# Kernel optimization log

Measured on AMD Instinct MI355X. Metric: run time of the kernel, lower is better.

## Reference

```python
import jax, jax.numpy as jnp
import numpy as np

T = 100      # sequence length / output times
B = 2048     # batch
DT = 0.02    # euler step == spacing of ts -> one step per interval
CLAMP = 6.0
LOG2PI = float(np.log(2.0 * np.pi))
sp = jax.nn.softplus


def setup_inputs() -> dict:
    key = jax.random.key(0)
    ks = jax.random.split(key, 20)
    rn = lambda k, s, sc=1.0: jax.random.normal(k, s, dtype=jnp.float32) * sc
    inp = {}
    inp['xs'] = rn(ks[0], (T, B, 3, 50))
    inp['ts'] = jnp.arange(T, dtype=jnp.float32) * DT
    inp['eps0'] = rn(ks[1], (B, 6))
    inp['dW'] = rn(ks[2], (T - 1, B, 6)) * np.sqrt(DT)  # Brownian increments ~ N(0, dt)
    # encoder: 150->30->30->15
    inp['eW1'] = rn(ks[3], (150, 30), 150 ** -0.5); inp['eb1'] = jnp.zeros((30,), jnp.float32)
    inp['eW2'] = rn(ks[4], (30, 30), 30 ** -0.5);   inp['eb2'] = jnp.zeros((30,), jnp.float32)
    inp['eW3'] = rn(ks[5], (30, 15), 30 ** -0.5);   inp['eb3'] = jnp.zeros((15,), jnp.float32)
    # decoder: 6->30->30->100
    inp['dcW1'] = rn(ks[6], (6, 30), 6 ** -0.5);    inp['dcb1'] = jnp.zeros((30,), jnp.float32)
    inp['dcW2'] = rn(ks[7], (30, 30), 30 ** -0.5);  inp['dcb2'] = jnp.zeros((30,), jnp.float32)
    inp['dcW3'] = rn(ks[8], (30, 100), 30 ** -0.5); inp['dcb3'] = jnp.zeros((100,), jnp.float32)
    # f_net: (6+1+3)=10 -> 30 -> 6
    inp['fW1'] = rn(ks[9], (10, 30), 10 ** -0.5);   inp['fb1'] = jnp.zeros((30,), jnp.float32)
    inp['fW2'] = rn(ks[10], (30, 6), 30 ** -0.5);   inp['fb2'] = jnp.zeros((6,), jnp.float32)
    # h_net: (6+1)=7 -> 30 -> 6
    inp['hW1'] = rn(ks[11], (7, 30), 7 ** -0.5);    inp['hb1'] = jnp.zeros((30,), jnp.float32)
    inp['hW2'] = rn(ks[12], (30, 6), 30 ** -0.5);   inp['hb2'] = jnp.zeros((6,), jnp.float32)
    # 6 g_nets stacked: 2 -> 30 -> 1 (sigmoid)
    inp['gW1'] = rn(ks[13], (6, 2, 30), 2 ** -0.5); inp['gb1'] = jnp.zeros((6, 30), jnp.float32)
    inp['gW2'] = rn(ks[14], (6, 30, 1), 30 ** -0.5); inp['gb2'] = jnp.zeros((6, 1), jnp.float32)
    inp['pz0_mean'] = jnp.zeros((1, 6), jnp.float32)
    inp['pz0_logstd'] = jnp.zeros((1, 6), jnp.float32)
    return inp


def _forward(xs, ts, eps0, dW, eW1, eb1, eW2, eb2, eW3, eb3,
             dcW1, dcb1, dcW2, dcb2, dcW3, dcb3,
             fW1, fb1, fW2, fb2, hW1, hb1, hW2, hb2,
             gW1, gb1, gW2, gb2, pz0_mean, pz0_logstd):
    # ---- encoder on time-reversed xs ----
    xse = jnp.flip(xs, 0).reshape(T, B, 150)
    e = sp(xse @ eW1 + eb1)
    e = sp(e @ eW2 + eb2)
    e = e @ eW3 + eb3                         # [T,B,15]
    qz0_mean = e[-1, :, :6]
    qz0_logstd = e[-1, :, 6:12]
    ctx = jnp.flip(e[..., 12:15], 0)           # [T,B,3]

    z0 = qz0_mean + jnp.exp(jnp.clip(qz0_logstd, -CLAMP, CLAMP)) * eps0

    # ---- Euler-Maruyama with logqp (one step per ts interval) ----
    def step(z, sc):
        k, dWk = sc
        t = ts[k]
        dtk = ts[k + 1] - ts[k]
        c = ctx[jnp.minimum(k + 1, T - 1)]     # searchsorted(ts, t, right=True) clamped
        tb = jnp.broadcast_to(t, (B, 1)).astype(z.dtype)
        f = sp(jnp.concatenate([tb, z, c], 1) @ fW1 + fb1) @ fW2 + fb2
        h = sp(jnp.concatenate([tb, z], 1) @ hW1 + hb1) @ hW2 + hb2
        gin = jnp.stack([jnp.broadcast_to(t, (B, 6)).astype(z.dtype), z], -1)  # [B,6,2]
        gh = sp(jnp.einsum('bdi,dih->bdh', gin, gW1) + gb1)
        g = jax.nn.sigmoid(jnp.einsum('bdh,dho->bdo', gh, gW2) + gb2)[..., 0]  # [B,6]
        u = (f - h) / g
        logr = 0.5 * jnp.sum(u * u, axis=1) * dtk   # [B]
        zn = z + f * dtk + g * dWk
        return zn, (zn, logr)

    _, (zs_tail, log_ratio) = jax.lax.scan(step, z0, (jnp.arange(T - 1), dW))
    zs = jnp.concatenate([z0[None], zs_tail], 0)   # [T,B,6]

    # ---- decoder + likelihood ----
    d = sp(zs @ dcW1 + dcb1)
    d = sp(d @ dcW2 + dcb2)
    d = d @ dcW3 + dcb3                        # [T,B,100]
    xm, xl = d[..., :50], d[..., 50:]
    xsig = jnp.exp(jnp.clip(xl, -CLAMP, CLAMP))
    tgt = xs[:, :, -1, :]
    lp = -0.5 * ((tgt - xm) / xsig) ** 2 - jnp.log(xsig) - 0.5 * LOG2PI
    log_pxs = jnp.mean(jnp.sum(lp, axis=(0, 2)))

    # ---- KL(q(z0)||p(z0)) + path term ----
    sq = jnp.exp(jnp.clip(qz0_logstd, -CLAMP, CLAMP))
    spz = jnp.exp(jnp.clip(pz0_logstd, -CLAMP, CLAMP))
    kl = jnp.log(spz / sq) + (sq ** 2 + (qz0_mean - pz0_mean) ** 2) / (2.0 * spz ** 2) - 0.5
    logqp0 = jnp.mean(jnp.sum(kl, axis=1))
    logqp_path = jnp.mean(jnp.sum(log_ratio, axis=0))
    return log_pxs, logqp0 + logqp_path


def reference(xs, ts, eps0, dW, eW1, eb1, eW2, eb2, eW3, eb3,
              dcW1, dcb1, dcW2, dcb2, dcW3, dcb3,
              fW1, fb1, fW2, fb2, hW1, hb1, hW2, hb2,
              gW1, gb1, gW2, gb2, pz0_mean, pz0_logstd):
    return _forward(xs, ts, eps0, dW, eW1, eb1, eW2, eb2, eW3, eb3,
                    dcW1, dcb1, dcW2, dcb2, dcW3, dcb3,
                    fW1, fb1, fW2, fb2, hW1, hb1, hW2, hb2,
                    gW1, gb1, gW2, gb2, pz0_mean, pz0_logstd)
```

## Files before the change

kernel.cpp:

```cpp
#include <hip/hip_runtime.h>
#include <hip/hip_bf16.h>
#include <math.h>

#define Tn 100
#define Bn 2048

typedef int v2i __attribute__((ext_vector_type(2)));

__device__ __forceinline__ float sp_f(float x) {
    float e = __expf(-fabsf(x));
    return fmaxf(x, 0.f) + __logf(1.f + e);
}
__device__ __forceinline__ float clamp6(float x) {
    return fminf(fmaxf(x, -6.f), 6.f);
}
__device__ __forceinline__ float dpp_xor1(float x) {
    return __int_as_float(__builtin_amdgcn_mov_dpp(__float_as_int(x), 0xB1, 0xF, 0xF, 1));
}
__device__ __forceinline__ float dpp_xor2(float x) {
    return __int_as_float(__builtin_amdgcn_mov_dpp(__float_as_int(x), 0x4E, 0xF, 0xF, 1));
}
__device__ __forceinline__ float dpp_hmirror(float x) {
    return __int_as_float(__builtin_amdgcn_mov_dpp(__float_as_int(x), 0x141, 0xF, 0xF, 1));
}
__device__ __forceinline__ float dpp_ror8(float x) {
    return __int_as_float(__builtin_amdgcn_mov_dpp(__float_as_int(x), 0x128, 0xF, 0xF, 1));
}
template <int OFF>
__device__ __forceinline__ float swz(float x) {
    return __int_as_float(__builtin_amdgcn_ds_swizzle(__float_as_int(x), OFF));
}
__device__ __forceinline__ float xor16_sum(float x) {
#if __has_builtin(__builtin_amdgcn_permlane16_swap)
    v2i r = __builtin_amdgcn_permlane16_swap(__float_as_int(x), __float_as_int(x), false, false);
    return __int_as_float(r[0]) + __int_as_float(r[1]);
#else
    return x + swz<0x401F>(x);
#endif
}
__device__ __forceinline__ float other_half(float x) {
#if __has_builtin(__builtin_amdgcn_permlane32_swap)
    v2i r = __builtin_amdgcn_permlane32_swap(__float_as_int(x), __float_as_int(x), false, false);
    return (__int_as_float(r[0]) + __int_as_float(r[1])) - x;
#else
    return __shfl_xor(x, 32);
#endif
}

__device__ __forceinline__ void row2(float* ha, float* hb, const float* wrow,
                                     float va, float vb) {
#pragma unroll
    for (int q = 0; q < 7; ++q) {
        float4 wv = *(const float4*)(wrow + 4 * q);
        ha[4 * q + 0] = fmaf(va, wv.x, ha[4 * q + 0]);
        hb[4 * q + 0] = fmaf(vb, wv.x, hb[4 * q + 0]);
        ha[4 * q + 1] = fmaf(va, wv.y, ha[4 * q + 1]);
        hb[4 * q + 1] = fmaf(vb, wv.y, hb[4 * q + 1]);
        ha[4 * q + 2] = fmaf(va, wv.z, ha[4 * q + 2]);
        hb[4 * q + 2] = fmaf(vb, wv.z, hb[4 * q + 2]);
        ha[4 * q + 3] = fmaf(va, wv.w, ha[4 * q + 3]);
        hb[4 * q + 3] = fmaf(vb, wv.w, hb[4 * q + 3]);
    }
    float2 wt = *(const float2*)(wrow + 28);
    ha[28] = fmaf(va, wt.x, ha[28]);
    hb[28] = fmaf(vb, wt.x, hb[28]);
    ha[29] = fmaf(va, wt.y, ha[29]);
    hb[29] = fmaf(vb, wt.y, hb[29]);
}
__device__ __forceinline__ void dot30_2(const float* ha, const float* hb,
                                        const float* wrow, float& ra, float& rb) {
    float a0 = 0.f, a1 = 0.f, b0 = 0.f, b1 = 0.f;
#pragma unroll
    for (int q = 0; q < 7; ++q) {
        float4 wv = *(const float4*)(wrow + 4 * q);
        a0 = fmaf(ha[4 * q + 0], wv.x, a0);
        b0 = fmaf(hb[4 * q + 0], wv.x, b0);
        a1 = fmaf(ha[4 * q + 1], wv.y, a1);
        b1 = fmaf(hb[4 * q + 1], wv.y, b1);
        a0 = fmaf(ha[4 * q + 2], wv.z, a0);
        b0 = fmaf(hb[4 * q + 2], wv.z, b0);
        a1 = fmaf(ha[4 * q + 3], wv.w, a1);
        b1 = fmaf(hb[4 * q + 3], wv.w, b1);
    }
    float2 wt = *(const float2*)(wrow + 28);
    a0 = fmaf(ha[28], wt.x, a0);
    b0 = fmaf(hb[28], wt.x, b0);
    a1 = fmaf(ha[29], wt.y, a1);
    b1 = fmaf(hb[29], wt.y, b1);
    ra = a0 + a1; rb = b0 + b1;
}

#define ENC_LOAD2(b0, b1, base)                                               \
    _Pragma("unroll")                                                         \
    for (int i = 0; i < 5; ++i) {                                             \
        b0[i] = *(const float2*)(x0 + (base) + 2 * i);                        \
        b1[i] = *(const float2*)(x1 + (base) + 2 * i);                        \
    }
#define ENC_COMP2(b0, b1, base)                                               \
    _Pragma("unroll")                                                         \
    for (int i = 0; i < 5; ++i) {                                             \
        row2(h1a, h1b, &w[(base + 2 * i) * 32], b0[i].x, b1[i].x);            \
        row2(h1a, h1b, &w[(base + 2 * i + 1) * 32], b0[i].y, b1[i].y);        \
    }

__global__ __launch_bounds__(256) void enc_kernel(
    const float* __restrict__ xs,
    const float* __restrict__ eW1, const float* __restrict__ eb1,
    const float* __restrict__ eW2, const float* __restrict__ eb2,
    const float* __restrict__ eW3, const float* __restrict__ eb3,
    float* __restrict__ ctx, float* __restrict__ qm, float* __restrict__ qs)
{
    __shared__ float w[6292];
    for (int i = threadIdx.x; i < 4500; i += 256) w[(i / 30) * 32 + (i % 30)] = eW1[i];
    if (threadIdx.x < 30) w[4800 + threadIdx.x] = eb1[threadIdx.x];
    for (int i = threadIdx.x; i < 900; i += 256) w[4832 + (i / 30) * 32 + (i % 30)] = eW2[i];
    if (threadIdx.x < 30) w[5792 + threadIdx.x] = eb2[threadIdx.x];
    for (int i = threadIdx.x; i < 450; i += 256) w[5824 + i] = eW3[i];
    if (threadIdx.x < 15) w[6274 + threadIdx.x] = eb3[threadIdx.x];
    __syncthreads();

    int t = threadIdx.x;
    size_t base = (size_t)blockIdx.x * 512;
    size_t s0 = base + t, s1 = base + t + 256;
    const float* x0 = xs + s0 * 150;
    const float* x1 = xs + s1 * 150;

    float h1a[30], h1b[30];
#pragma unroll
    for (int j = 0; j < 30; ++j) { h1a[j] = w[4800 + j]; h1b[j] = h1a[j]; }

    float2 A0[5], A1[5], B0[5], B1[5];
    ENC_LOAD2(A0, A1, 0)
    ENC_LOAD2(B0, B1, 10)
    int fb = 0;
#pragma unroll 1
    for (int it = 0; it < 6; ++it) {
        ENC_COMP2(A0, A1, fb)
        ENC_LOAD2(A0, A1, fb + 20)
        ENC_COMP2(B0, B1, fb + 10)
        ENC_LOAD2(B0, B1, fb + 30)
        fb += 20;
    }
    ENC_COMP2(A0, A1, 120)
    ENC_LOAD2(A0, A1, 140)
    ENC_COMP2(B0, B1, 130)
    ENC_COMP2(A0, A1, 140)

#pragma unroll
    for (int j = 0; j < 30; ++j) { h1a[j] = sp_f(h1a[j]); h1b[j] = sp_f(h1b[j]); }

    float h2a[30], h2b[30];
#pragma unroll
    for (int j = 0; j < 30; ++j) { h2a[j] = w[5792 + j]; h2b[j] = h2a[j]; }
#pragma unroll
    for (int j1 = 0; j1 < 30; ++j1)
        row2(h2a, h2b, &w[4832 + j1 * 32], h1a[j1], h1b[j1]);
#pragma unroll
    for (int j = 0; j < 30; ++j) { h2a[j] = sp_f(h2a[j]); h2b[j] = sp_f(h2b[j]); }

    float oa12 = w[6274 + 12], oa13 = w[6274 + 13], oa14 = w[6274 + 14];
    float ob12 = oa12, ob13 = oa13, ob14 = oa14;
#pragma unroll
    for (int j2 = 0; j2 < 30; ++j2) {
        float w12 = w[5824 + j2 * 15 + 12];
        float w13 = w[5824 + j2 * 15 + 13];
        float w14 = w[5824 + j2 * 15 + 14];
        oa12 = fmaf(h2a[j2], w12, oa12); ob12 = fmaf(h2b[j2], w12, ob12);
        oa13 = fmaf(h2a[j2], w13, oa13); ob13 = fmaf(h2b[j2], w13, ob13);
        oa14 = fmaf(h2a[j2], w14, oa14); ob14 = fmaf(h2b[j2], w14, ob14);
    }
    float* cp0 = ctx + s0 * 3;
    cp0[0] = oa12; cp0[1] = oa13; cp0[2] = oa14;
    float* cp1 = ctx + s1 * 3;
    cp1[0] = ob12; cp1[1] = ob13; cp1[2] = ob14;

    if (blockIdx.x < 4) {
        float oa[12], ob[12];
#pragma unroll
        for (int j3 = 0; j3 < 12; ++j3) { oa[j3] = w[6274 + j3]; ob[j3] = oa[j3]; }
#pragma unroll
        for (int j2 = 0; j2 < 30; ++j2) {
            float hva = h2a[j2], hvb = h2b[j2];
#pragma unroll
            for (int j3 = 0; j3 < 12; ++j3) {
                float wv = w[5824 + j2 * 15 + j3];
                oa[j3] = fmaf(hva, wv, oa[j3]);
                ob[j3] = fmaf(hvb, wv, ob[j3]);
            }
        }
#pragma unroll
        for (int d = 0; d < 6; ++d) {
            qm[s0 * 6 + d] = oa[d]; qs[s0 * 6 + d] = oa[6 + d];
            qm[s1 * 6 + d] = ob[d]; qs[s1 * 6 + d] = ob[6 + d];
        }
    }
}

__global__ __launch_bounds__(128, 4) void scan_kernel(
    const float* __restrict__ ts, const float* __restrict__ dWall,
    const float* __restrict__ fW1, const float* __restrict__ fb1,
    const float* __restrict__ fW2, const float* __restrict__ fb2,
    const float* __restrict__ hW1, const float* __restrict__ hb1,
    const float* __restrict__ hW2, const float* __restrict__ hb2,
    const float* __restrict__ gW1, const float* __restrict__ gb1,
    const float* __restrict__ gW2, const float* __restrict__ gb2,
    const float* __restrict__ ctx,
    const float* __restrict__ qm, const float* __restrict__ qs,
    const float* __restrict__ eps0, const float* __restrict__ pm,
    const float* __restrict__ ps,
    float* __restrict__ zsb, float* __restrict__ acc)
{
    int tid = threadIdx.x;
    int lane = tid & 63;
    int b = blockIdx.x;
    bool isA = tid < 64;

    __shared__ float sRec[99 * 12];
    __shared__ float exF[2][12];
    __shared__ float exG[2][8];

    for (int i = tid; i < 99 * 3; i += 128) {
        int k = i / 3, e = i % 3;
        float2 v = *(const float2*)(dWall + ((size_t)k * Bn + b) * 6 + e * 2);
        *(float2*)&sRec[k * 12 + e * 2] = v;
    }
    for (int i = tid; i < 99 * 3; i += 128) {
        int k = i / 3, e = i % 3;
        sRec[k * 12 + 6 + e] = ctx[((size_t)(k + 1) * Bn + b) * 3 + e];
    }
    for (int i = tid; i < 99; i += 128) {
        float t0 = ts[i], t1 = ts[i + 1];
        sRec[i * 12 + 9]  = 0.f;
        sRec[i * 12 + 10] = t0;
        sRec[i * 12 + 11] = t1 - t0;
    }

    float z[6];
    float zq = 0.f;
    float wl1[10], b1w, wl2[6], fb2v[6], hb2v[6];
    float gwa[4], gwb[4], gw2v[4], gbb[4], gb2v = 0.f, wselq = 0.f;
    int dL = 0;

    if (isA) {
        bool lower = lane < 32;
        int j = lane & 31;
        int jc = (j < 30) ? j : 29;
        bool jvalid = (j < 30);
#pragma unroll
        for (int i = 0; i < 10; ++i)
            wl1[i] = lower ? fW1[i * 30 + jc] : (i < 7 ? hW1[i * 30 + jc] : 0.f);
        b1w = lower ? fb1[jc] : hb1[jc];
#pragma unroll
        for (int d = 0; d < 6; ++d)
            wl2[d] = jvalid ? (lower ? fW2[jc * 6 + d] : hW2[jc * 6 + d]) : 0.f;
#pragma unroll
        for (int d = 0; d < 6; ++d) { fb2v[d] = fb2[d]; hb2v[d] = hb2[d]; }
#pragma unroll
        for (int d = 0; d < 6; ++d) {
            float m = qm[b * 6 + d];
            float sq = __expf(clamp6(qs[b * 6 + d]));
            z[d] = fmaf(sq, eps0[b * 6 + d], m);
        }
        if (tid == 0) {
            float* zp = zsb + (size_t)b * 6;
            *(float2*)(zp)     = make_float2(z[0], z[1]);
            *(float2*)(zp + 2) = make_float2(z[2], z[3]);
            *(float2*)(zp + 4) = make_float2(z[4], z[5]);
        }
    } else {
        int dL8 = lane >> 3;
        dL = (dL8 < 6) ? dL8 : 0;
        wselq = (dL8 < 6) ? 0.0625f : 0.f;
        int s = lane & 7;
#pragma unroll
        for (int u = 0; u < 4; ++u) {
            int jj = s + 8 * u;
            bool ok = (dL8 < 6) && (jj < 30);
            gwa[u]  = ok ? gW1[dL * 60 + jj] : 0.f;
            gwb[u]  = ok ? gW1[dL * 60 + 30 + jj] : 0.f;
            gw2v[u] = ok ? gW2[dL * 30 + jj] : 0.f;
            gbb[u]  = ok ? gb1[dL * 30 + jj] : 0.f;
        }
        gb2v = gb2[dL];
        {
            float m = qm[b * 6 + dL];
            float sq = __expf(clamp6(qs[b * 6 + dL]));
            zq = fmaf(sq, eps0[b * 6 + dL], m);
        }
        if (tid == 64) {
            float klsum = 0.f;
#pragma unroll
            for (int d = 0; d < 6; ++d) {
                float m = qm[b * 6 + d];
                float sq = __expf(clamp6(qs[b * 6 + d]));
                float spz = __expf(clamp6(ps[d]));
                float dm = m - pm[d];
                klsum += __logf(spz / sq) + (sq * sq + dm * dm) / (2.f * spz * spz) - 0.5f;
            }
            atomicAdd(&acc[1], klsum);
        }
    }

    __syncthreads();

    float pacc = 0.f;

    for (int k = 0; k < Tn - 1; ++k) {
        int kb = k & 1;

        if (isA) {
            float4 r0 = *(float4*)&sRec[k * 12];
            float4 r1 = *(float4*)&sRec[k * 12 + 4];
            float4 r2 = *(float4*)&sRec[k * 12 + 8];
            float t = r2.z, dt = r2.w;

            float a = fmaf(t, wl1[0], b1w);
#pragma unroll
            for (int i = 0; i < 6; ++i) a = fmaf(z[i], wl1[1 + i], a);
            a = fmaf(r1.z, wl1[7], a);
            a = fmaf(r1.w, wl1[8], a);
            a = fmaf(r2.x, wl1[9], a);
            float hid = sp_f(a);

            float pp[6];
#pragma unroll
            for (int d = 0; d < 6; ++d) pp[d] = hid * wl2[d];
#pragma unroll
            for (int d = 0; d < 6; ++d) pp[d] += dpp_xor1(pp[d]);
#pragma unroll
            for (int d = 0; d < 6; ++d) pp[d] += dpp_xor2(pp[d]);
#pragma unroll
            for (int d = 0; d < 6; ++d) pp[d] += dpp_hmirror(pp[d]);
#pragma unroll
            for (int d = 0; d < 6; ++d) pp[d] += dpp_ror8(pp[d]);
#pragma unroll
            for (int d = 0; d < 6; ++d) pp[d] = xor16_sum(pp[d]);
            float fvv[6], dfh[6];
            bool lower = lane < 32;
#pragma unroll
            for (int d = 0; d < 6; ++d) {
                float oth = other_half(pp[d]);
                float fsum = lower ? pp[d] : oth;
                float hsum = lower ? oth : pp[d];
                fvv[d] = fsum + fb2v[d];
                dfh[d] = fvv[d] - (hsum + hb2v[d]);
            }
            if (lane == 0) {
                *(float4*)&exF[kb][0] = make_float4(fvv[0], fvv[1], fvv[2], fvv[3]);
                *(float4*)&exF[kb][4] = make_float4(fvv[4], fvv[5], dfh[0], dfh[1]);
                *(float4*)&exF[kb][8] = make_float4(dfh[2], dfh[3], dfh[4], dfh[5]);
            }

            __syncthreads();

            float4 g03 = *(float4*)&exG[kb][0];
            float2 g45 = *(float2*)&exG[kb][4];
            float gl[6] = { g03.x, g03.y, g03.z, g03.w, g45.x, g45.y };
            float dwv[6] = { r0.x, r0.y, r0.z, r0.w, r1.x, r1.y };
#pragma unroll
            for (int d = 0; d < 6; ++d)
                z[d] = fmaf(gl[d], dwv[d], fmaf(fvv[d], dt, z[d]));

            if (tid == 0) {
                float* zp = zsb + ((size_t)(k + 1) * Bn + b) * 6;
                *(float2*)(zp)     = make_float2(z[0], z[1]);
                *(float2*)(zp + 2) = make_float2(z[2], z[3]);
                *(float2*)(zp + 4) = make_float2(z[4], z[5]);
            }
        } else {
            float2 tdt = *(float2*)&sRec[k * 12 + 10];
            float t = tdt.x, dt = tdt.y;
            float dwq = sRec[k * 12 + dL];

            float ga = 0.f;
#pragma unroll
            for (int u = 0; u < 4; ++u) {
                float pre = fmaf(t, gwa[u], gbb[u]);
                pre = fmaf(zq, gwb[u], pre);
                ga = fmaf(sp_f(pre), gw2v[u], ga);
            }
            ga += dpp_xor1(ga);
            ga += dpp_xor2(ga);
            ga += dpp_hmirror(ga);
            float gacc = ga + gb2v;
            float e = __expf(-gacc);
            float rg = 1.f + e;
            float gval = __builtin_amdgcn_rcpf(rg);
            if ((lane & 7) == 0 && (lane >> 3) < 6)
                exG[kb][dL] = gval;

            __syncthreads();

            float fq  = exF[kb][dL];
            float dfq = exF[kb][6 + dL];
            float u = dfq * rg;
            pacc = fmaf(wselq * dt, u * u, pacc);
            zq = fmaf(gval, dwq, fmaf(fq, dt, zq));
        }
    }
    if (!isA) {
#pragma unroll
        for (int mm = 1; mm <= 32; mm <<= 1) pacc += __shfl_xor(pacc, mm);
        if (tid == 64) atomicAdd(&acc[2], pacc);
    }
}

#define DEC_TLOAD(b0, b1, base)                                               \
    _Pragma("unroll")                                                         \
    for (int i = 0; i < 5; ++i) {                                             \
        b0[i] = *(const float2*)(tg0 + (base) + 2 * i);                       \
        b1[i] = *(const float2*)(tg1 + (base) + 2 * i);                       \
    }
#define DEC_LCOMP(b0, b1, base)                                               \
    _Pragma("unroll")                                                         \
    for (int i = 0; i < 10; ++i) {                                            \
        int ff = (base) + i;                                                  \
        float dma, dmb, dla, dlb;                                             \
        dot30_2(h2a, h2b, &w[1216 + ff * 32], dma, dmb);                      \
        dot30_2(h2a, h2b, &w[1216 + (50 + ff) * 32], dla, dlb);               \
        float xma = w[4416 + ff] + dma, xmb = w[4416 + ff] + dmb;             \
        float cla = clamp6(w[4416 + 50 + ff] + dla);                          \
        float clb = clamp6(w[4416 + 50 + ff] + dlb);                          \
        float tva = (i & 1) ? b0[i >> 1].y : b0[i >> 1].x;                    \
        float tvb = (i & 1) ? b1[i >> 1].y : b1[i >> 1].x;                    \
        float ua = (tva - xma) * __expf(-cla);                                \
        float ub = (tvb - xmb) * __expf(-clb);                                \
        lpa += -0.5f * ua * ua - cla - 0.91893853320467274f;                  \
        lpb += -0.5f * ub * ub - clb - 0.91893853320467274f;                  \
    }

__global__ __launch_bounds__(256) void dec_kernel(
    const float* __restrict__ zsb, const float* __restrict__ xs,
    const float* __restrict__ dcW1, const float* __restrict__ dcb1,
    const float* __restrict__ dcW2, const float* __restrict__ dcb2,
    const float* __restrict__ dcW3, const float* __restrict__ dcb3,
    float* __restrict__ acc)
{
    __shared__ float w[4516];
    for (int i = threadIdx.x; i < 180; i += 256) w[(i / 30) * 32 + (i % 30)] = dcW1[i];
    if (threadIdx.x < 30) w[192 + threadIdx.x] = dcb1[threadIdx.x];
    for (int i = threadIdx.x; i < 900; i += 256) w[224 + (i / 30) * 32 + (i % 30)] = dcW2[i];
    if (threadIdx.x < 30) w[1184 + threadIdx.x] = dcb2[threadIdx.x];
    for (int i = threadIdx.x; i < 3000; i += 256) {
        int j2 = i / 100, j3 = i % 100;
        w[1216 + j3 * 32 + j2] = dcW3[i];
    }
    for (int i = threadIdx.x; i < 100; i += 256) w[4416 + i] = dcb3[i];
    __syncthreads();

    int t = threadIdx.x;
    size_t base = (size_t)blockIdx.x * 512;
    size_t s0 = base + t, s1 = base + t + 256;

    float za[6], zb[6];
    {
        const float* zp0 = zsb + s0 * 6;
        const float* zp1 = zsb + s1 * 6;
#pragma unroll
        for (int i = 0; i < 3; ++i) {
            float2 v0 = *(const float2*)(zp0 + 2 * i);
            float2 v1 = *(const float2*)(zp1 + 2 * i);
            za[2 * i] = v0.x; za[2 * i + 1] = v0.y;
            zb[2 * i] = v1.x; zb[2 * i + 1] = v1.y;
        }
    }

    float h1a[30], h1b[30];
#pragma unroll
    for (int j = 0; j < 30; ++j) { h1a[j] = w[192 + j]; h1b[j] = h1a[j]; }
#pragma unroll
    for (int i = 0; i < 6; ++i) row2(h1a, h1b, &w[i * 32], za[i], zb[i]);
#pragma unroll
    for (int j = 0; j < 30; ++j) { h1a[j] = sp_f(h1a[j]); h1b[j] = sp_f(h1b[j]); }

    float h2a[30], h2b[30];
#pragma unroll
    for (int j = 0; j < 30; ++j) { h2a[j] = w[1184 + j]; h2b[j] = h2a[j]; }
#pragma unroll
    for (int j1 = 0; j1 < 30; ++j1)
        row2(h2a, h2b, &w[224 + j1 * 32], h1a[j1], h1b[j1]);
#pragma unroll
    for (int j = 0; j < 30; ++j) { h2a[j] = sp_f(h2a[j]); h2b[j] = sp_f(h2b[j]); }

    const float* tg0 = xs + s0 * 150 + 100;
    const float* tg1 = xs + s1 * 150 + 100;
    float lpa = 0.f, lpb = 0.f;
    float2 TA0[5], TA1[5], TB0[5], TB1[5];
    DEC_TLOAD(TA0, TA1, 0)
    DEC_TLOAD(TB0, TB1, 10)
    DEC_LCOMP(TA0, TA1, 0)
    DEC_TLOAD(TA0, TA1, 20)
    DEC_LCOMP(TB0, TB1, 10)
    DEC_TLOAD(TB0, TB1, 30)
    DEC_LCOMP(TA0, TA1, 20)
    DEC_TLOAD(TA0, TA1, 40)
    DEC_LCOMP(TB0, TB1, 30)
    DEC_LCOMP(TA0, TA1, 40)

    float lpacc = lpa + lpb;
#pragma unroll
    for (int mm = 1; mm <= 32; mm <<= 1) lpacc += __shfl_xor(lpacc, mm);
    __shared__ float red[4];
    if ((threadIdx.x & 63) == 0) red[threadIdx.x >> 6] = lpacc;
    __syncthreads();
    if (threadIdx.x == 0) atomicAdd(&acc[0], red[0] + red[1] + red[2] + red[3]);
}

__global__ void final_kernel(const float* __restrict__ acc, float* __restrict__ out)
{
    out[0] = acc[0] * (1.f / (float)Bn);
    out[1] = (acc[1] + acc[2]) * (1.f / (float)Bn);
}

extern "C" void kernel_launch(void* const* d_in, const int* in_sizes, int n_in,
                              void* d_out, int out_size, void* d_ws, size_t ws_size,
                              hipStream_t stream)
{
    const float* xs   = (const float*)d_in[0];
    const float* ts   = (const float*)d_in[1];
    const float* eps0 = (const float*)d_in[2];
    const float* dW   = (const float*)d_in[3];
    const float* eW1  = (const float*)d_in[4];
    const float* eb1  = (const float*)d_in[5];
    const float* eW2  = (const float*)d_in[6];
    const float* eb2  = (const float*)d_in[7];
    const float* eW3  = (const float*)d_in[8];
    const float* eb3  = (const float*)d_in[9];
    const float* dcW1 = (const float*)d_in[10];
    const float* dcb1 = (const float*)d_in[11];
    const float* dcW2 = (const float*)d_in[12];
    const float* dcb2 = (const float*)d_in[13];
    const float* dcW3 = (const float*)d_in[14];
    const float* dcb3 = (const float*)d_in[15];
    const float* fW1  = (const float*)d_in[16];
    const float* fb1  = (const float*)d_in[17];
    const float* fW2  = (const float*)d_in[18];
    const float* fb2  = (const float*)d_in[19];
    const float* hW1  = (const float*)d_in[20];
    const float* hb1  = (const float*)d_in[21];
    const float* hW2  = (const float*)d_in[22];
    const float* hb2  = (const float*)d_in[23];
    const float* gW1  = (const float*)d_in[24];
    const float* gb1  = (const float*)d_in[25];
    const float* gW2  = (const float*)d_in[26];
    const float* gb2  = (const float*)d_in[27];
    const float* pm   = (const float*)d_in[28];
    const float* ps   = (const float*)d_in[29];

    float* ws  = (float*)d_ws;
    float* acc = ws;
    float* ctx = ws + 16;
    float* qm  = ctx + 614400;
    float* qs  = qm + 12288;
    float* zs  = qs + 12288;
    float* out = (float*)d_out;

    hipMemsetAsync(acc, 0, 16 * sizeof(float), stream);
    enc_kernel<<<400, 256, 0, stream>>>(xs, eW1, eb1, eW2, eb2, eW3, eb3, ctx, qm, qs);
    scan_kernel<<<2048, 128, 0, stream>>>(ts, dW, fW1, fb1, fW2, fb2, hW1, hb1,
                                          hW2, hb2, gW1, gb1, gW2, gb2, ctx,
                                          qm, qs, eps0, pm, ps, zs, acc);
    dec_kernel<<<400, 256, 0, stream>>>(zs, xs, dcW1, dcb1, dcW2, dcb2, dcW3, dcb3, acc);
    final_kernel<<<1, 1, 0, stream>>>(acc, out);
}
```

Before: 253.5 us.

## Use packed fp16 dot2 instructions for encoder and decoder MLP layers

Packs encoder and decoder weights and activations into fp16 pairs and replaces the fp32 FMA matrix products with v_dot2 fp16 instructions that accumulate in fp32, which halves the instruction count of the large layers. Shared memory layouts are rebuilt to hold the packed weights, and the encoder output layer is reorganised into dot products over transposed rows. This cuts ALU work and LDS traffic in the per-sample MLPs, at the cost of fp16 rounding of inputs, weights and hidden activations, which could push numerical error past tolerance.

Measured after the change: 244.0 us (median of 2 runs). 3.7% less time.

```diff
diff --git a/kernel.cpp b/kernel.cpp
--- a/kernel.cpp
+++ b/kernel.cpp
@@ -6,6 +6,7 @@
 #define Bn 2048
 
 typedef int v2i __attribute__((ext_vector_type(2)));
+typedef _Float16 h2v __attribute__((ext_vector_type(2)));
 
 __device__ __forceinline__ float sp_f(float x) {
     float e = __expf(-fabsf(x));
@@ -14,6 +15,20 @@
 __device__ __forceinline__ float clamp6(float x) {
     return fminf(fmaxf(x, -6.f), 6.f);
 }
+__device__ __forceinline__ unsigned int packh2(float a, float b) {
+    h2v h; h.x = (_Float16)a; h.y = (_Float16)b;
+    return __builtin_bit_cast(unsigned int, h);
+}
+__device__ __forceinline__ float dot2f(unsigned int a, unsigned int b, float c) {
+#if __has_builtin(__builtin_amdgcn_fdot2)
+    return __builtin_amdgcn_fdot2(__builtin_bit_cast(h2v, a),
+                                  __builtin_bit_cast(h2v, b), c, false);
+#else
+    h2v ha = __builtin_bit_cast(h2v, a), hb = __builtin_bit_cast(h2v, b);
+    return fmaf((float)ha.y, (float)hb.y, fmaf((float)ha.x, (float)hb.x, c));
+#endif
+}
+
 __device__ __forceinline__ float dpp_xor1(float x) {
     return __int_as_float(__builtin_amdgcn_mov_dpp(__float_as_int(x), 0xB1, 0xF, 0xF, 1));
 }
@@ -47,25 +62,25 @@
 #endif
 }
 
-__device__ __forceinline__ void row2(float* ha, float* hb, const float* wrow,
-                                     float va, float vb) {
+__device__ __forceinline__ void rowd2(float* ha, float* hb, const unsigned int* wrow,
+                                      unsigned int xa, unsigned int xb) {
 #pragma unroll
     for (int q = 0; q < 7; ++q) {
-        float4 wv = *(const float4*)(wrow + 4 * q);
-        ha[4 * q + 0] = fmaf(va, wv.x, ha[4 * q + 0]);
-        hb[4 * q + 0] = fmaf(vb, wv.x, hb[4 * q + 0]);
-        ha[4 * q + 1] = fmaf(va, wv.y, ha[4 * q + 1]);
-        hb[4 * q + 1] = fmaf(vb, wv.y, hb[4 * q + 1]);
-        ha[4 * q + 2] = fmaf(va, wv.z, ha[4 * q + 2]);
-        hb[4 * q + 2] = fmaf(vb, wv.z, hb[4 * q + 2]);
-        ha[4 * q + 3] = fmaf(va, wv.w, ha[4 * q + 3]);
-        hb[4 * q + 3] = fmaf(vb, wv.w, hb[4 * q + 3]);
-    }
-    float2 wt = *(const float2*)(wrow + 28);
-    ha[28] = fmaf(va, wt.x, ha[28]);
-    hb[28] = fmaf(vb, wt.x, hb[28]);
-    ha[29] = fmaf(va, wt.y, ha[29]);
-    hb[29] = fmaf(vb, wt.y, hb[29]);
+        uint4 wv = *(const uint4*)(wrow + 4 * q);
+        ha[4 * q + 0] = dot2f(xa, wv.x, ha[4 * q + 0]);
+        hb[4 * q + 0] = dot2f(xb, wv.x, hb[4 * q + 0]);
+        ha[4 * q + 1] = dot2f(xa, wv.y, ha[4 * q + 1]);
+        hb[4 * q + 1] = dot2f(xb, wv.y, hb[4 * q + 1]);
+        ha[4 * q + 2] = dot2f(xa, wv.z, ha[4 * q + 2]);
+        hb[4 * q + 2] = dot2f(xb, wv.z, hb[4 * q + 2]);
+        ha[4 * q + 3] = dot2f(xa, wv.w, ha[4 * q + 3]);
+        hb[4 * q + 3] = dot2f(xb, wv.w, hb[4 * q + 3]);
+    }
+    uint2 wt = *(const uint2*)(wrow + 28);
+    ha[28] = dot2f(xa, wt.x, ha[28]);
+    hb[28] = dot2f(xb, wt.x, hb[28]);
+    ha[29] = dot2f(xa, wt.y, ha[29]);
+    hb[29] = dot2f(xb, wt.y, hb[29]);
 }
 __device__ __forceinline__ void dot30_2(const float* ha, const float* hb,
                                         const float* wrow, float& ra, float& rb) {
@@ -89,6 +104,23 @@
     b1 = fmaf(hb[29], wt.y, b1);
     ra = a0 + a1; rb = b0 + b1;
 }
+__device__ __forceinline__ void dot16p_2(const unsigned int* pa, const unsigned int* pb,
+                                         const unsigned int* wrow, float& ra, float& rb) {
+    float a0 = 0.f, a1 = 0.f, b0 = 0.f, b1 = 0.f;
+#pragma unroll
+    for (int q = 0; q < 4; ++q) {
+        uint4 wv = *(const uint4*)(wrow + 4 * q);
+        a0 = dot2f(pa[4 * q + 0], wv.x, a0);
+        b0 = dot2f(pb[4 * q + 0], wv.x, b0);
+        a1 = dot2f(pa[4 * q + 1], wv.y, a1);
+        b1 = dot2f(pb[4 * q + 1], wv.y, b1);
+        a0 = dot2f(pa[4 * q + 2], wv.z, a0);
+        b0 = dot2f(pb[4 * q + 2], wv.z, b0);
+        a1 = dot2f(pa[4 * q + 3], wv.w, a1);
+        b1 = dot2f(pb[4 * q + 3], wv.w, b1);
+    }
+    ra = a0 + a1; rb = b0 + b1;
+}
 
 #define ENC_LOAD2(b0, b1, base)                                               \
     _Pragma("unroll")                                                         \
@@ -96,11 +128,12 @@
         b0[i] = *(const float2*)(x0 + (base) + 2 * i);                        \
         b1[i] = *(const float2*)(x1 + (base) + 2 * i);                        \
     }
-#define ENC_COMP2(b0, b1, base)                                               \
+#define ENC_COMP2(b0, b1, pb)                                                 \
     _Pragma("unroll")                                                         \
     for (int i = 0; i < 5; ++i) {                                             \
-        row2(h1a, h1b, &w[(base + 2 * i) * 32], b0[i].x, b1[i].x);            \
-        row2(h1a, h1b, &w[(base + 2 * i + 1) * 32], b0[i].y, b1[i].y);        \
+        unsigned int xa = packh2(b0[i].x, b0[i].y);                           \
+        unsigned int xb = packh2(b1[i].x, b1[i].y);                           \
+        rowd2(h1a, h1b, &wh1[((pb) + i) * 32], xa, xb);                       \
     }
 
 __global__ __launch_bounds__(256) void enc_kernel(
@@ -110,13 +143,29 @@
     const float* __restrict__ eW3, const float* __restrict__ eb3,
     float* __restrict__ ctx, float* __restrict__ qm, float* __restrict__ qs)
 {
-    __shared__ float w[6292];
-    for (int i = threadIdx.x; i < 4500; i += 256) w[(i / 30) * 32 + (i % 30)] = eW1[i];
-    if (threadIdx.x < 30) w[4800 + threadIdx.x] = eb1[threadIdx.x];
-    for (int i = threadIdx.x; i < 900; i += 256) w[4832 + (i / 30) * 32 + (i % 30)] = eW2[i];
-    if (threadIdx.x < 30) w[5792 + threadIdx.x] = eb2[threadIdx.x];
-    for (int i = threadIdx.x; i < 450; i += 256) w[5824 + i] = eW3[i];
-    if (threadIdx.x < 15) w[6274 + threadIdx.x] = eb3[threadIdx.x];
+    __shared__ __align__(16) unsigned int wh1[75 * 32];
+    __shared__ __align__(16) unsigned int wh2[15 * 32];
+    __shared__ __align__(16) float wf[555];
+
+    for (int i = threadIdx.x; i < 75 * 30; i += 256) {
+        int p = i / 30, j = i % 30;
+        wh1[p * 32 + j] = packh2(eW1[(2 * p) * 30 + j], eW1[(2 * p + 1) * 30 + j]);
+    }
+    for (int i = threadIdx.x; i < 15 * 30; i += 256) {
+        int p = i / 30, j = i % 30;
+        wh2[p * 32 + j] = packh2(eW2[(2 * p) * 30 + j], eW2[(2 * p + 1) * 30 + j]);
+    }
+    if (threadIdx.x < 30) wf[threadIdx.x] = eb1[threadIdx.x];
+    if (threadIdx.x >= 32 && threadIdx.x < 62) wf[30 + threadIdx.x - 32] = eb2[threadIdx.x - 32];
+    for (int i = threadIdx.x; i < 90; i += 256) {
+        int o = i / 30, j2 = i % 30;
+        wf[60 + o * 32 + j2] = eW3[j2 * 15 + 12 + o];
+    }
+    for (int i = threadIdx.x; i < 360; i += 256) {
+        int o = i / 30, j2 = i % 30;
+        wf[156 + o * 32 + j2] = eW3[j2 * 15 + o];
+    }
+    if (threadIdx.x >= 64 && threadIdx.x < 79) wf[540 + threadIdx.x - 64] = eb3[threadIdx.x - 64];
     __syncthreads();
 
     int t = threadIdx.x;
@@ -127,7 +176,7 @@
 
     float h1a[30], h1b[30];
 #pragma unroll
-    for (int j = 0; j < 30; ++j) { h1a[j] = w[4800 + j]; h1b[j] = h1a[j]; }
+    for (int j = 0; j < 30; ++j) { h1a[j] = wf[j]; h1b[j] = h1a[j]; }
 
     float2 A0[5], A1[5], B0[5], B1[5];
     ENC_LOAD2(A0, A1, 0)
@@ -135,63 +184,56 @@
     int fb = 0;
 #pragma unroll 1
     for (int it = 0; it < 6; ++it) {
-        ENC_COMP2(A0, A1, fb)
+        ENC_COMP2(A0, A1, fb / 2)
         ENC_LOAD2(A0, A1, fb + 20)
-        ENC_COMP2(B0, B1, fb + 10)
+        ENC_COMP2(B0, B1, fb / 2 + 5)
         ENC_LOAD2(B0, B1, fb + 30)
         fb += 20;
     }
-    ENC_COMP2(A0, A1, 120)
+    ENC_COMP2(A0, A1, 60)
     ENC_LOAD2(A0, A1, 140)
-    ENC_COMP2(B0, B1, 130)
-    ENC_COMP2(A0, A1, 140)
+    ENC_COMP2(B0, B1, 65)
+    ENC_COMP2(A0, A1, 70)
 
 #pragma unroll
     for (int j = 0; j < 30; ++j) { h1a[j] = sp_f(h1a[j]); h1b[j] = sp_f(h1b[j]); }
 
+    unsigned int p1a[15], p1b[15];
+#pragma unroll
+    for (int p = 0; p < 15; ++p) {
+        p1a[p] = packh2(h1a[2 * p], h1a[2 * p + 1]);
+        p1b[p] = packh2(h1b[2 * p], h1b[2 * p + 1]);
+    }
     float h2a[30], h2b[30];
 #pragma unroll
-    for (int j = 0; j < 30; ++j) { h2a[j] = w[5792 + j]; h2b[j] = h2a[j]; }
-#pragma unroll
-    for (int j1 = 0; j1 < 30; ++j1)
-        row2(h2a, h2b, &w[4832 + j1 * 32], h1a[j1], h1b[j1]);
+    for (int j = 0; j < 30; ++j) { h2a[j] = wf[30 + j]; h2b[j] = h2a[j]; }
+#pragma unroll
+    for (int p = 0; p < 15; ++p)
+        rowd2(h2a, h2b, &wh2[p * 32], p1a[p], p1b[p]);
 #pragma unroll
     for (int j = 0; j < 30; ++j) { h2a[j] = sp_f(h2a[j]); h2b[j] = sp_f(h2b[j]); }
 
-    float oa12 = w[6274 + 12], oa13 = w[6274 + 13], oa14 = w[6274 + 14];
-    float ob12 = oa12, ob13 = oa13, ob14 = oa14;
-#pragma unroll
-    for (int j2 = 0; j2 < 30; ++j2) {
-        float w12 = w[5824 + j2 * 15 + 12];
-        float w13 = w[5824 + j2 * 15 + 13];
-        float w14 = w[5824 + j2 * 15 + 14];
-        oa12 = fmaf(h2a[j2], w12, oa12); ob12 = fmaf(h2b[j2], w12, ob12);
-        oa13 = fmaf(h2a[j2], w13, oa13); ob13 = fmaf(h2b[j2], w13, ob13);
-        oa14 = fmaf(h2a[j2], w14, oa14); ob14 = fmaf(h2b[j2], w14, ob14);
+    float oa3[3], ob3[3];
+#pragma unroll
+    for (int o = 0; o < 3; ++o) {
+        float ra, rb;
+        dot30_2(h2a, h2b, &wf[60 + o * 32], ra, rb);
+        oa3[o] = wf[540 + 12 + o] + ra;
+        ob3[o] = wf[540 + 12 + o] + rb;
     }
     float* cp0 = ctx + s0 * 3;
-    cp0[0] = oa12; cp0[1] = oa13; cp0[2] = oa14;
+    cp0[0] = oa3[0]; cp0[1] = oa3[1]; cp0[2] = oa3[2];
     float* cp1 = ctx + s1 * 3;
-    cp1[0] = ob12; cp1[1] = ob13; cp1[2] = ob14;
+    cp1[0] = ob3[0]; cp1[1] = ob3[1]; cp1[2] = ob3[2];
 
     if (blockIdx.x < 4) {
-        float oa[12], ob[12];
-#pragma unroll
-        for (int j3 = 0; j3 < 12; ++j3) { oa[j3] = w[6274 + j3]; ob[j3] = oa[j3]; }
-#pragma unroll
-        for (int j2 = 0; j2 < 30; ++j2) {
-            float hva = h2a[j2], hvb = h2b[j2];
-#pragma unroll
-            for (int j3 = 0; j3 < 12; ++j3) {
-                float wv = w[5824 + j2 * 15 + j3];
-                oa[j3] = fmaf(hva, wv, oa[j3]);
-                ob[j3] = fmaf(hvb, wv, ob[j3]);
-            }
-        }
-#pragma unroll
-        for (int d = 0; d < 6; ++d) {
-            qm[s0 * 6 + d] = oa[d]; qs[s0 * 6 + d] = oa[6 + d];
-            qm[s1 * 6 + d] = ob[d]; qs[s1 * 6 + d] = ob[6 + d];
+#pragma unroll
+        for (int o = 0; o < 12; ++o) {
+            float ra, rb;
+            dot30_2(h2a, h2b, &wf[156 + o * 32], ra, rb);
+            float va = wf[540 + o] + ra, vb = wf[540 + o] + rb;
+            if (o < 6) { qm[s0 * 6 + o] = va; qm[s1 * 6 + o] = vb; }
+            else       { qs[s0 * 6 + o - 6] = va; qs[s1 * 6 + o - 6] = vb; }
         }
     }
 }
@@ -416,11 +458,11 @@
     for (int i = 0; i < 10; ++i) {                                            \
         int ff = (base) + i;                                                  \
         float dma, dmb, dla, dlb;                                             \
-        dot30_2(h2a, h2b, &w[1216 + ff * 32], dma, dmb);                      \
-        dot30_2(h2a, h2b, &w[1216 + (50 + ff) * 32], dla, dlb);               \
-        float xma = w[4416 + ff] + dma, xmb = w[4416 + ff] + dmb;             \
-        float cla = clamp6(w[4416 + 50 + ff] + dla);                          \
-        float clb = clamp6(w[4416 + 50 + ff] + dlb);                          \
+        dot16p_2(p2a, p2b, &wh3[ff * 16], dma, dmb);                          \
+        dot16p_2(p2a, p2b, &wh3[(50 + ff) * 16], dla, dlb);                   \
+        float xma = wd[256 + ff] + dma, xmb = wd[256 + ff] + dmb;             \
+        float cla = clamp6(wd[256 + 50 + ff] + dla);                          \
+        float clb = clamp6(wd[256 + 50 + ff] + dlb);                          \
         float tva = (i & 1) ? b0[i >> 1].y : b0[i >> 1].x;                    \
         float tvb = (i & 1) ? b1[i >> 1].y : b1[i >> 1].x;                    \
         float ua = (tva - xma) * __expf(-cla);                                \
@@ -436,16 +478,22 @@
     const float* __restrict__ dcW3, const float* __restrict__ dcb3,
     float* __restrict__ acc)
 {
-    __shared__ float w[4516];
-    for (int i = threadIdx.x; i < 180; i += 256) w[(i / 30) * 32 + (i % 30)] = dcW1[i];
-    if (threadIdx.x < 30) w[192 + threadIdx.x] = dcb1[threadIdx.x];
-    for (int i = threadIdx.x; i < 900; i += 256) w[224 + (i / 30) * 32 + (i % 30)] = dcW2[i];
-    if (threadIdx.x < 30) w[1184 + threadIdx.x] = dcb2[threadIdx.x];
-    for (int i = threadIdx.x; i < 3000; i += 256) {
-        int j2 = i / 100, j3 = i % 100;
-        w[1216 + j3 * 32 + j2] = dcW3[i];
-    }
-    for (int i = threadIdx.x; i < 100; i += 256) w[4416 + i] = dcb3[i];
+    __shared__ __align__(16) float wd[356];
+    __shared__ __align__(16) unsigned int wh2d[15 * 32];
+    __shared__ __align__(16) unsigned int wh3[100 * 16];
+
+    for (int i = threadIdx.x; i < 180; i += 256) wd[(i / 30) * 32 + (i % 30)] = dcW1[i];
+    if (threadIdx.x < 30) wd[192 + threadIdx.x] = dcb1[threadIdx.x];
+    if (threadIdx.x >= 32 && threadIdx.x < 62) wd[224 + threadIdx.x - 32] = dcb2[threadIdx.x - 32];
+    for (int i = threadIdx.x; i < 100; i += 256) wd[256 + i] = dcb3[i];
+    for (int i = threadIdx.x; i < 15 * 30; i += 256) {
+        int p = i / 30, j = i % 30;
+        wh2d[p * 32 + j] = packh2(dcW2[(2 * p) * 30 + j], dcW2[(2 * p + 1) * 30 + j]);
+    }
+    for (int i = threadIdx.x; i < 100 * 16; i += 256) {
+        int ff = i / 16, p = i % 16;
+        wh3[i] = (p < 15) ? packh2(dcW3[(2 * p) * 100 + ff], dcW3[(2 * p + 1) * 100 + ff]) : 0u;
+    }
     __syncthreads();
 
     int t = threadIdx.x;
@@ -467,20 +515,54 @@
 
     float h1a[30], h1b[30];
 #pragma unroll
-    for (int j = 0; j < 30; ++j) { h1a[j] = w[192 + j]; h1b[j] = h1a[j]; }
-#pragma unroll
-    for (int i = 0; i < 6; ++i) row2(h1a, h1b, &w[i * 32], za[i], zb[i]);
+    for (int j = 0; j < 30; ++j) { h1a[j] = wd[192 + j]; h1b[j] = h1a[j]; }
+#pragma unroll
+    for (int i = 0; i < 6; ++i) {
+        float via = za[i], vib = zb[i];
+        const float* wrow = &wd[i * 32];
+#pragma unroll
+        for (int q = 0; q < 7; ++q) {
+            float4 wv = *(const float4*)(wrow + 4 * q);
+            h1a[4 * q + 0] = fmaf(via, wv.x, h1a[4 * q + 0]);
+            h1b[4 * q + 0] = fmaf(vib, wv.x, h1b[4 * q + 0]);
+            h1a[4 * q + 1] = fmaf(via, wv.y, h1a[4 * q + 1]);
+            h1b[4 * q + 1] = fmaf(vib, wv.y, h1b[4 * q + 1]);
+            h1a[4 * q + 2] = fmaf(via, wv.z, h1a[4 * q + 2]);
+            h1b[4 * q + 2] = fmaf(vib, wv.z, h1b[4 * q + 2]);
+            h1a[4 * q + 3] = fmaf(via, wv.w, h1a[4 * q + 3]);
+            h1b[4 * q + 3] = fmaf(vib, wv.w, h1b[4 * q + 3]);
+        }
+        float2 wt = *(const float2*)(wrow + 28);
+        h1a[28] = fmaf(via, wt.x, h1a[28]);
+        h1b[28] = fmaf(vib, wt.x, h1b[28]);
+        h1a[29] = fmaf(via, wt.y, h1a[29]);
+        h1b[29] = fmaf(vib, wt.y, h1b[29]);
+    }
 #pragma unroll
     for (int j = 0; j < 30; ++j) { h1a[j] = sp_f(h1a[j]); h1b[j] = sp_f(h1b[j]); }
 
+    unsigned int p1a[15], p1b[15];
+#pragma unroll
+    for (int p = 0; p < 15; ++p) {
+        p1a[p] = packh2(h1a[2 * p], h1a[2 * p + 1]);
+        p1b[p] = packh2(h1b[2 * p], h1b[2 * p + 1]);
+    }
     float h2a[30], h2b[30];
 #pragma unroll
-    for (int j = 0; j < 30; ++j) { h2a[j] = w[1184 + j]; h2b[j] = h2a[j]; }
-#pragma unroll
-    for (int j1 = 0; j1 < 30; ++j1)
-        row2(h2a, h2b, &w[224 + j1 * 32], h1a[j1], h1b[j1]);
+    for (int j = 0; j < 30; ++j) { h2a[j] = wd[224 + j]; h2b[j] = h2a[j]; }
+#pragma unroll
+    for (int p = 0; p < 15; ++p)
+        rowd2(h2a, h2b, &wh2d[p * 32], p1a[p], p1b[p]);
 #pragma unroll
     for (int j = 0; j < 30; ++j) { h2a[j] = sp_f(h2a[j]); h2b[j] = sp_f(h2b[j]); }
+
+    unsigned int p2a[16], p2b[16];
+#pragma unroll
+    for (int p = 0; p < 15; ++p) {
+        p2a[p] = packh2(h2a[2 * p], h2a[2 * p + 1]);
+        p2b[p] = packh2(h2b[2 * p], h2b[2 * p + 1]);
+    }
+    p2a[15] = 0u; p2b[15] = 0u;
 
     const float* tg0 = xs + s0 * 150 + 100;
     const float* tg1 = xs + s1 * 150 + 100;
```
